# Kernel tuning notes

Measured on AMD Instinct MI355X. Metric: run time of the kernel, lower is better.

Reference implementation:

```python
import jax, jax.numpy as jnp
import numpy as np

C = 256
NH = 8
G = 32  # groupnorm groups (min(32, C))
EPS = 1e-6


def setup_inputs() -> dict:
    key = jax.random.key(0)
    ks = jax.random.split(key, 7)
    B, D, H, W = 2, 16, 16, 16
    x = jax.random.normal(ks[0], (B, C, D, H, W), dtype=jnp.float32)
    gn_gamma = jnp.ones((C,), jnp.float32)
    gn_beta = jnp.zeros((C,), jnp.float32)
    s = 1.0 / np.sqrt(C)
    qkv_w = jax.random.normal(ks[1], (3 * C, C), jnp.float32) * s  # 1x1x1 conv weight
    qkv_b = jnp.zeros((3 * C,), jnp.float32)
    proj_w = jax.random.normal(ks[2], (C, C), jnp.float32) * s
    proj_b = jnp.zeros((C,), jnp.float32)
    return {"x": x, "gn_gamma": gn_gamma, "gn_beta": gn_beta,
            "qkv_w": qkv_w, "qkv_b": qkv_b, "proj_w": proj_w, "proj_b": proj_b}


def _group_norm(x, gamma, beta):
    # x: [B, C, S]
    B, Cc, S = x.shape
    xg = x.reshape(B, G, (Cc // G) * S)
    mu = xg.mean(axis=-1, keepdims=True)
    var = xg.var(axis=-1, keepdims=True)
    xg = (xg - mu) * jax.lax.rsqrt(var + EPS)
    x = xg.reshape(B, Cc, S)
    return x * gamma[None, :, None] + beta[None, :, None]


def reference(x, gn_gamma, gn_beta, qkv_w, qkv_b, proj_w, proj_b):
    B, Cc, D, H, W = x.shape
    S = D * H * W
    hd = Cc // NH
    xf = x.reshape(B, Cc, S)
    h = _group_norm(xf, gn_gamma, gn_beta)
    # 1x1x1 conv == channel matmul: [B, 3C, S]
    qkv = jnp.einsum('oc,bcs->bos', qkv_w, h) + qkv_b[None, :, None]
    # torch path: reshape(B,3C,S).permute(0,2,1).chunk -> q=channels[0:C]
    q, k, v = qkv[:, :Cc], qkv[:, Cc:2 * Cc], qkv[:, 2 * Cc:]
    # [B, C, S] -> [B, NH, S, hd]
    def to_heads(t):
        return t.reshape(B, NH, hd, S).transpose(0, 1, 3, 2)
    q, k, v = to_heads(q), to_heads(k), to_heads(v)
    scale = hd ** (-0.5)
    attn = jax.nn.softmax(jnp.einsum('bnqd,bnkd->bnqk', q, k) * scale, axis=-1)
    o = jnp.einsum('bnqk,bnkd->bnqd', attn, v)  # [B, NH, S, hd]
    o = o.transpose(0, 1, 3, 2).reshape(B, Cc, S)  # back to [B, C, S]
    o = jnp.einsum('oc,bcs->bos', proj_w, o) + proj_b[None, :, None]
    return x + o.reshape(B, Cc, D, H, W)
```

## Files before the change

kernel.cpp:

```cpp
#include <hip/hip_runtime.h>
#include <cstddef>

#define S_LEN 4096
#define C_DIM 256
#define NHEADS 8
#define HDIM 32

typedef __attribute__((ext_vector_type(8))) _Float16 half8;
typedef __attribute__((ext_vector_type(4))) _Float16 half4;
typedef __attribute__((ext_vector_type(2))) _Float16 h2t;
typedef __attribute__((ext_vector_type(2))) __fp16 fp16x2;
typedef __attribute__((ext_vector_type(4))) float floatx4;

#define SC2F ((float)(0.17677669529663687 * 1.4426950408889634))

__global__ __launch_bounds__(256) void prep_stats(
    const float* __restrict__ qkv_w, const float* __restrict__ proj_w,
    const float* __restrict__ qkv_b, const float* __restrict__ x,
    _Float16* __restrict__ wq, _Float16* __restrict__ wp,
    float* __restrict__ qbias, float* __restrict__ pstat)
{
  const int blk = blockIdx.x;
  const int tid = threadIdx.x;
  if (blk < 512) {
    __shared__ float red[2][4];
    const int gb = blk >> 3, e = blk & 7;
    const int g = gb & 31, b = gb >> 5;
    const float* xb = x + ((size_t)b * C_DIM + g * 8) * S_LEN + e * 4096;
    const float4* x4 = (const float4*)xb;
    float sum = 0.f, sumsq = 0.f;
    #pragma unroll
    for (int i = 0; i < 4; ++i) {
      float4 v = x4[tid + i * 256];
      sum += v.x + v.y + v.z + v.w;
      sumsq += v.x * v.x + v.y * v.y + v.z * v.z + v.w * v.w;
    }
    for (int off = 1; off < 64; off <<= 1) {
      sum += __shfl_xor(sum, off, 64);
      sumsq += __shfl_xor(sumsq, off, 64);
    }
    const int wv = tid >> 6, lane = tid & 63;
    if (lane == 0) { red[0][wv] = sum; red[1][wv] = sumsq; }
    __syncthreads();
    if (tid == 0) {
      pstat[(gb * 8 + e) * 2 + 0] = red[0][0] + red[0][1] + red[0][2] + red[0][3];
      pstat[(gb * 8 + e) * 2 + 1] = red[1][0] + red[1][1] + red[1][2] + red[1][3];
    }
  } else {
    int idx = (blk - 512) * 256 + tid;
    if (idx < 768 * 256) {
      float v = qkv_w[idx];
      if (idx < 256 * 256) v *= SC2F;
      wq[idx] = (_Float16)v;
    } else if (idx < 768 * 256 + 256 * 256) {
      int i = idx - 768 * 256;
      wp[i] = (_Float16)proj_w[i];
    } else if (idx < 768 * 256 + 256 * 256 + 768) {
      int i = idx - (768 * 256 + 256 * 256);
      float bv = qkv_b[i];
      if (i < 256) bv *= SC2F;
      qbias[i] = bv;
    }
  }
}

__global__ __launch_bounds__(256) void qkv_gn_gemm(
    const _Float16* __restrict__ W, const float* __restrict__ bias,
    const float* __restrict__ x, const float* __restrict__ gamma,
    const float* __restrict__ beta, const float* __restrict__ pstat,
    _Float16* __restrict__ qo, _Float16* __restrict__ ko_,
    _Float16* __restrict__ vo)
{
  __shared__ __align__(16) _Float16 Ld[64 * 264];
  const int tid = threadIdx.x;
  const int b = blockIdx.z;
  const int s0 = blockIdx.y * 64;

  {
    const int c0 = (tid & 127) * 2, c1 = c0 + 1;
    const int sh = tid >> 7;
    const int g = c0 >> 3;
    const int gb = b * 32 + g;
    float s = 0.f, sq = 0.f;
    #pragma unroll
    for (int e = 0; e < 8; ++e) {
      s  += pstat[(gb * 8 + e) * 2 + 0];
      sq += pstat[(gb * 8 + e) * 2 + 1];
    }
    const float mean = s * (1.f / 32768.f);
    const float rstd = rsqrtf(sq * (1.f / 32768.f) - mean * mean + 1e-6f);
    const float ga0 = gamma[c0] * rstd, be0 = beta[c0] - mean * ga0;
    const float ga1 = gamma[c1] * rstd, be1 = beta[c1] - mean * ga1;
    const float4* xa = (const float4*)(x + ((size_t)b * C_DIM + c0) * S_LEN + s0 + sh * 32);
    const float4* xc = (const float4*)(x + ((size_t)b * C_DIM + c1) * S_LEN + s0 + sh * 32);
    #pragma unroll
    for (int j = 0; j < 8; ++j) {
      float4 a = xa[j], c = xc[j];
      int sl = sh * 32 + j * 4;
      *(h2t*)&Ld[(sl + 0) * 264 + c0] = (h2t){ (_Float16)(a.x * ga0 + be0), (_Float16)(c.x * ga1 + be1) };
      *(h2t*)&Ld[(sl + 1) * 264 + c0] = (h2t){ (_Float16)(a.y * ga0 + be0), (_Float16)(c.y * ga1 + be1) };
      *(h2t*)&Ld[(sl + 2) * 264 + c0] = (h2t){ (_Float16)(a.z * ga0 + be0), (_Float16)(c.z * ga1 + be1) };
      *(h2t*)&Ld[(sl + 3) * 264 + c0] = (h2t){ (_Float16)(a.w * ga0 + be0), (_Float16)(c.w * ga1 + be1) };
    }
  }
  __syncthreads();

  const int lane = tid & 63, wv = tid >> 6;
  const int m = lane & 15, quad = lane >> 4;
  const int mtb = blockIdx.x * 8 + wv * 2;
  const _Float16* wrow0 = W + (size_t)((mtb + 0) * 16 + m) * C_DIM + quad * 8;
  const _Float16* wrow1 = W + (size_t)((mtb + 1) * 16 + m) * C_DIM + quad * 8;
  const _Float16* lp = &Ld[m * 264 + quad * 8];

  floatx4 acc[2][4];
  #pragma unroll
  for (int j = 0; j < 2; ++j)
    #pragma unroll
    for (int s = 0; s < 4; ++s) acc[j][s] = (floatx4){0.f,0.f,0.f,0.f};

  #pragma unroll
  for (int k0 = 0; k0 < C_DIM; k0 += 32) {
    half8 b0 = *(const half8*)(lp + k0);
    half8 b1 = *(const half8*)(lp + 16 * 264 + k0);
    half8 b2 = *(const half8*)(lp + 32 * 264 + k0);
    half8 b3 = *(const half8*)(lp + 48 * 264 + k0);
    half8 a0 = *(const half8*)(wrow0 + k0);
    half8 a1 = *(const half8*)(wrow1 + k0);
    acc[0][0] = __builtin_amdgcn_mfma_f32_16x16x32_f16(a0, b0, acc[0][0], 0, 0, 0);
    acc[0][1] = __builtin_amdgcn_mfma_f32_16x16x32_f16(a0, b1, acc[0][1], 0, 0, 0);
    acc[0][2] = __builtin_amdgcn_mfma_f32_16x16x32_f16(a0, b2, acc[0][2], 0, 0, 0);
    acc[0][3] = __builtin_amdgcn_mfma_f32_16x16x32_f16(a0, b3, acc[0][3], 0, 0, 0);
    acc[1][0] = __builtin_amdgcn_mfma_f32_16x16x32_f16(a1, b0, acc[1][0], 0, 0, 0);
    acc[1][1] = __builtin_amdgcn_mfma_f32_16x16x32_f16(a1, b1, acc[1][1], 0, 0, 0);
    acc[1][2] = __builtin_amdgcn_mfma_f32_16x16x32_f16(a1, b2, acc[1][2], 0, 0, 0);
    acc[1][3] = __builtin_amdgcn_mfma_f32_16x16x32_f16(a1, b3, acc[1][3], 0, 0, 0);
  }

  if (blockIdx.x < 4) {
    #pragma unroll
    for (int j = 0; j < 2; ++j) {
      const int ob = (mtb + j) * 16 + quad * 4;
      const float bv0 = bias[ob], bv1 = bias[ob + 1],
                  bv2 = bias[ob + 2], bv3 = bias[ob + 3];
      #pragma unroll
      for (int sub = 0; sub < 4; ++sub) {
        int s = s0 + sub * 16 + m;
        half4 h = { (_Float16)(acc[j][sub][0] + bv0), (_Float16)(acc[j][sub][1] + bv1),
                    (_Float16)(acc[j][sub][2] + bv2), (_Float16)(acc[j][sub][3] + bv3) };
        _Float16* dst = (ob < 256) ? qo : ko_;
        int oo = ob & 255, n = oo >> 5, d0 = oo & 31;
        *(half4*)(dst + (((size_t)b * NHEADS + n) * S_LEN + s) * HDIM + d0) = h;
      }
    }
  } else {
    __syncthreads();
    _Float16* VLd = Ld;
    #pragma unroll
    for (int j = 0; j < 2; ++j) {
      const int ob = (mtb + j) * 16 + quad * 4;
      const int lch = (wv * 2 + j) * 16 + quad * 4;
      const float bv0 = bias[ob], bv1 = bias[ob + 1],
                  bv2 = bias[ob + 2], bv3 = bias[ob + 3];
      #pragma unroll
      for (int sub = 0; sub < 4; ++sub) {
        int s = sub * 16 + m;
        VLd[(lch + 0) * 72 + s] = (_Float16)(acc[j][sub][0] + bv0);
        VLd[(lch + 1) * 72 + s] = (_Float16)(acc[j][sub][1] + bv1);
        VLd[(lch + 2) * 72 + s] = (_Float16)(acc[j][sub][2] + bv2);
        VLd[(lch + 3) * 72 + s] = (_Float16)(acc[j][sub][3] + bv3);
      }
    }
    __syncthreads();
    const int lch = tid >> 1, sh = tid & 1;
    const int oo = (blockIdx.x - 4) * 128 + lch;
    const int n = oo >> 5, d = oo & 31;
    _Float16* dst = vo + ((size_t)(b * NHEADS + n) * HDIM + d) * S_LEN + s0 + sh * 32;
    const _Float16* src = VLd + lch * 72 + sh * 32;
    *(half8*)(dst + 0)  = *(const half8*)(src + 0);
    *(half8*)(dst + 8)  = *(const half8*)(src + 8);
    *(half8*)(dst + 16) = *(const half8*)(src + 16);
    *(half8*)(dst + 24) = *(const half8*)(src + 24);
  }
}

__global__ __launch_bounds__(512) void attn_kernel(
    const _Float16* __restrict__ q, const _Float16* __restrict__ k,
    const _Float16* __restrict__ v, _Float16* __restrict__ po,
    float* __restrict__ pl)
{
  __shared__ __align__(16) _Float16 Kl[2][128 * 40];
  __shared__ __align__(16) _Float16 Vl[2][32 * 136];
  const int tid = threadIdx.x;
  const int lane = tid & 63, wv = tid >> 6;
  const int m = lane & 15, quad = lane >> 4;
  const int n = blockIdx.y, b = blockIdx.z;
  const int qc = blockIdx.x >> 1, kh = blockIdx.x & 1;
  const int q0 = qc * 256 + wv * 32;
  const int bh = b * NHEADS + n;

  const _Float16* qb = q + (size_t)bh * S_LEN * HDIM;
  const _Float16* kb = k + (size_t)bh * S_LEN * HDIM + (size_t)kh * 2048 * HDIM;
  const _Float16* vb = v + (size_t)bh * HDIM * S_LEN + (size_t)kh * 2048;

  half8 qfA = *(const half8*)(qb + (size_t)(q0 + m) * HDIM + quad * 8);
  half8 qfB = *(const half8*)(qb + (size_t)(q0 + 16 + m) * HDIM + quad * 8);

  const int krow = wv * 16 + (lane >> 2), kc = (lane & 3) * 8;
  const int vrow = wv * 4 + (lane >> 4), vc = (lane & 15) * 8;
  const _Float16* kg = kb + (size_t)krow * HDIM + kc;
  const _Float16* vg = vb + (size_t)vrow * S_LEN + vc;
  const int klds = krow * 40 + kc;
  const int vlds = vrow * 136 + vc;

  int4 kreg = *(const int4*)kg;
  int4 vreg = *(const int4*)vg;
  const _Float16* kgp = kg + 128 * HDIM;
  const _Float16* vgp = vg + 128;

  floatx4 oA0 = {0.f,0.f,0.f,0.f}, oA1 = oA0, oB0 = oA0, oB1 = oA0;
  float lA0 = 0.f, lA1 = 0.f, lB0 = 0.f, lB1 = 0.f;
  const fp16x2 one2 = { (__fp16)1.0f, (__fp16)1.0f };
  const floatx4 zz = {0.f,0.f,0.f,0.f};

  #pragma unroll 2
  for (int it = 0; it < 16; ++it) {
    const int bufi = it & 1;
    *(int4*)(&Kl[bufi][klds]) = kreg;
    *(int4*)(&Vl[bufi][vlds]) = vreg;
    kreg = *(const int4*)kgp; kgp += 128 * HDIM;
    vreg = *(const int4*)vgp; vgp += 128;
    __syncthreads();
    const _Float16* Kb = Kl[bufi];
    const _Float16* Vb = Vl[bufi];

    #pragma unroll
    for (int t = 0; t < 8; ++t) {
      const int tt = (t + wv) & 7;
      half8 kf  = *(const half8*)(Kb + (tt * 16 + m) * 40 + quad * 8);
      half4 vf0 = *(const half4*)(Vb + m * 136 + tt * 16 + quad * 4);
      half4 vf1 = *(const half4*)(Vb + (16 + m) * 136 + tt * 16 + quad * 4);
      __builtin_amdgcn_s_setprio(1);
      floatx4 sA = __builtin_amdgcn_mfma_f32_16x16x32_f16(kf, qfA, zz, 0, 0, 0);
      floatx4 sB = __builtin_amdgcn_mfma_f32_16x16x32_f16(kf, qfB, zz, 0, 0, 0);
      __builtin_amdgcn_s_setprio(0);
      float eA0 = __builtin_amdgcn_exp2f(sA[0]);
      float eA1 = __builtin_amdgcn_exp2f(sA[1]);
      float eA2 = __builtin_amdgcn_exp2f(sA[2]);
      float eA3 = __builtin_amdgcn_exp2f(sA[3]);
      float eB0 = __builtin_amdgcn_exp2f(sB[0]);
      float eB1 = __builtin_amdgcn_exp2f(sB[1]);
      float eB2 = __builtin_amdgcn_exp2f(sB[2]);
      float eB3 = __builtin_amdgcn_exp2f(sB[3]);
      half4 pA, pB;
      fp16x2 pAlo = __builtin_amdgcn_cvt_pkrtz(eA0, eA1);
      fp16x2 pAhi = __builtin_amdgcn_cvt_pkrtz(eA2, eA3);
      fp16x2 pBlo = __builtin_amdgcn_cvt_pkrtz(eB0, eB1);
      fp16x2 pBhi = __builtin_amdgcn_cvt_pkrtz(eB2, eB3);
      *(fp16x2*)&pA = pAlo; *((fp16x2*)&pA + 1) = pAhi;
      *(fp16x2*)&pB = pBlo; *((fp16x2*)&pB + 1) = pBhi;
      lA0 = __builtin_amdgcn_fdot2(pAlo, one2, lA0, false);
      lA1 = __builtin_amdgcn_fdot2(pAhi, one2, lA1, false);
      lB0 = __builtin_amdgcn_fdot2(pBlo, one2, lB0, false);
      lB1 = __builtin_amdgcn_fdot2(pBhi, one2, lB1, false);
      __builtin_amdgcn_s_setprio(1);
      oA0 = __builtin_amdgcn_mfma_f32_16x16x16f16(vf0, pA, oA0, 0, 0, 0);
      oA1 = __builtin_amdgcn_mfma_f32_16x16x16f16(vf1, pA, oA1, 0, 0, 0);
      oB0 = __builtin_amdgcn_mfma_f32_16x16x16f16(vf0, pB, oB0, 0, 0, 0);
      oB1 = __builtin_amdgcn_mfma_f32_16x16x16f16(vf1, pB, oB1, 0, 0, 0);
      __builtin_amdgcn_s_setprio(0);
    }
  }
  float lA = lA0 + lA1, lB = lB0 + lB1;
  lA += __shfl_xor(lA, 16, 64); lA += __shfl_xor(lA, 32, 64);
  lB += __shfl_xor(lB, 16, 64); lB += __shfl_xor(lB, 32, 64);
  _Float16* pobase = po + (size_t)kh * 2097152 + ((size_t)bh * S_LEN) * HDIM;
  {
    _Float16* poh = pobase + (size_t)(q0 + m) * HDIM;
    half4 h0 = { (_Float16)oA0[0], (_Float16)oA0[1], (_Float16)oA0[2], (_Float16)oA0[3] };
    half4 h1 = { (_Float16)oA1[0], (_Float16)oA1[1], (_Float16)oA1[2], (_Float16)oA1[3] };
    *(half4*)(poh + quad * 4) = h0;
    *(half4*)(poh + 16 + quad * 4) = h1;
    if (quad == 0) pl[(size_t)kh * 65536 + (size_t)bh * S_LEN + q0 + m] = lA;
  }
  {
    _Float16* poh = pobase + (size_t)(q0 + 16 + m) * HDIM;
    half4 h0 = { (_Float16)oB0[0], (_Float16)oB0[1], (_Float16)oB0[2], (_Float16)oB0[3] };
    half4 h1 = { (_Float16)oB1[0], (_Float16)oB1[1], (_Float16)oB1[2], (_Float16)oB1[3] };
    *(half4*)(poh + quad * 4) = h0;
    *(half4*)(poh + 16 + quad * 4) = h1;
    if (quad == 0) pl[(size_t)kh * 65536 + (size_t)bh * S_LEN + q0 + 16 + m] = lB;
  }
}

__global__ __launch_bounds__(256) void proj_gemm(
    const _Float16* __restrict__ W, const float* __restrict__ bias,
    const _Float16* __restrict__ po, const float* __restrict__ pl,
    const float* __restrict__ x, float* __restrict__ out)
{
  __shared__ float Linv[512];
  const int tid = threadIdx.x;
  const int lane = tid & 63, wv = tid >> 6;
  const int m = lane & 15, quad = lane >> 4;
  const int mt = blockIdx.x * 4 + wv;
  const int s0 = blockIdx.y * 64;
  const int b = blockIdx.z;
  const int row = mt * 16 + m;

  {
    const int nn = tid >> 5, jj = (tid & 31) * 2;
    size_t base = (size_t)(b * NHEADS + nn) * S_LEN + s0 + jj;
    float a0 = pl[base]     + pl[65536 + base];
    float a1 = pl[base + 1] + pl[65536 + base + 1];
    Linv[nn * 64 + jj]     = 1.f / a0;
    Linv[nn * 64 + jj + 1] = 1.f / a1;
  }
  __syncthreads();

  const _Float16* wrow = W + (size_t)row * C_DIM + quad * 8;
  floatx4 acc0 = {0.f,0.f,0.f,0.f}, acc1 = acc0, acc2 = acc0, acc3 = acc0;
  #pragma unroll
  for (int k0 = 0; k0 < C_DIM; k0 += 32) {
    const int n = k0 >> 5;
    const int d0 = quad * 8;
    half8 bf[4];
    #pragma unroll
    for (int sub = 0; sub < 4; ++sub) {
      size_t idx = (((size_t)(b * NHEADS + n)) * S_LEN + s0 + sub * 16 + m) * HDIM + d0;
      half8 a = *(const half8*)(po + idx);
      half8 c = *(const half8*)(po + 2097152 + idx);
      _Float16 iv = (_Float16)Linv[n * 64 + sub * 16 + m];
      bf[sub] = (a + c) * iv;
    }
    half8 af = *(const half8*)(wrow + k0);
    acc0 = __builtin_amdgcn_mfma_f32_16x16x32_f16(af, bf[0], acc0, 0, 0, 0);
    acc1 = __builtin_amdgcn_mfma_f32_16x16x32_f16(af, bf[1], acc1, 0, 0, 0);
    acc2 = __builtin_amdgcn_mfma_f32_16x16x32_f16(af, bf[2], acc2, 0, 0, 0);
    acc3 = __builtin_amdgcn_mfma_f32_16x16x32_f16(af, bf[3], acc3, 0, 0, 0);
  }
  floatx4 accs[4] = {acc0, acc1, acc2, acc3};
  #pragma unroll
  for (int sub = 0; sub < 4; ++sub) {
    int s = s0 + sub * 16 + m;
    #pragma unroll
    for (int r = 0; r < 4; ++r) {
      int c = mt * 16 + quad * 4 + r;
      size_t idx = ((size_t)b * C_DIM + c) * S_LEN + s;
      out[idx] = x[idx] + accs[sub][r] + bias[c];
    }
  }
}

extern "C" void kernel_launch(void* const* d_in, const int* in_sizes, int n_in,
                              void* d_out, int out_size, void* d_ws, size_t ws_size,
                              hipStream_t stream) {
  const float* x        = (const float*)d_in[0];
  const float* gn_gamma = (const float*)d_in[1];
  const float* gn_beta  = (const float*)d_in[2];
  const float* qkv_w    = (const float*)d_in[3];
  const float* qkv_b    = (const float*)d_in[4];
  const float* proj_w   = (const float*)d_in[5];
  const float* proj_b   = (const float*)d_in[6];
  float* out = (float*)d_out;

  const size_t n1 = (size_t)2 * S_LEN * C_DIM;
  char* ws = (char*)d_ws;
  _Float16* qx  = (_Float16*)ws;
  _Float16* kx  = qx + n1;
  _Float16* vx  = kx + n1;
  _Float16* wq  = vx + n1;
  _Float16* wp  = wq + 768 * 256;
  float*    qbias = (float*)(wp + 256 * 256);
  float*    pstat = qbias + 768;
  _Float16* po  = (_Float16*)(pstat + 1024);
  float*    pl  = (float*)(po + 2 * n1);

  prep_stats<<<1539, 256, 0, stream>>>(qkv_w, proj_w, qkv_b, x, wq, wp, qbias, pstat);
  qkv_gn_gemm<<<dim3(6, 64, 2), 256, 0, stream>>>(wq, qbias, x, gn_gamma, gn_beta, pstat, qx, kx, vx);
  attn_kernel<<<dim3(32, 8, 2), 512, 0, stream>>>(qx, kx, vx, po, pl);
  proj_gemm<<<dim3(4, 64, 2), 256, 0, stream>>>(wp, proj_b, po, pl, x, out);
}
```

Baseline: 148.3 us.

## Split GroupNorm into a transpose kernel and widen the QKV and proj GEMM tiles

GroupNorm normalisation and the fp16 transpose move into a new xnorm kernel that writes an [S,C] fp16 buffer. The QKV GEMM then only copies that buffer into LDS and computes 64 output rows per wave, halving its x-dimension grid. The output projection also doubles rows per wave, so each loaded po tile is reused across two weight tiles. The aim is to cut the redundant per-block recomputation of the normalised input (previously repeated in six blocks per tile) and to improve operand reuse. The cost is an extra kernel launch, a global round trip for the normalised activations, and fewer blocks with higher register pressure in both GEMMs.

```diff
diff --git a/kernel.cpp b/kernel.cpp
--- a/kernel.cpp
+++ b/kernel.cpp
@@ -64,91 +64,108 @@
   }
 }
 
-__global__ __launch_bounds__(256) void qkv_gn_gemm(
-    const _Float16* __restrict__ W, const float* __restrict__ bias,
+__global__ __launch_bounds__(256) void xnorm(
     const float* __restrict__ x, const float* __restrict__ gamma,
     const float* __restrict__ beta, const float* __restrict__ pstat,
+    _Float16* __restrict__ xt)
+{
+  __shared__ _Float16 Lt[16][264];
+  const int tid = threadIdx.x;
+  const int b = blockIdx.y;
+  const int s0 = blockIdx.x * 16;
+  const int c = tid;
+  const int gb = b * 32 + (c >> 3);
+  float s = 0.f, sq = 0.f;
+  #pragma unroll
+  for (int e = 0; e < 8; ++e) {
+    s  += pstat[(gb * 8 + e) * 2 + 0];
+    sq += pstat[(gb * 8 + e) * 2 + 1];
+  }
+  const float mean = s * (1.f / 32768.f);
+  const float rstd = rsqrtf(sq * (1.f / 32768.f) - mean * mean + 1e-6f);
+  const float ga = gamma[c] * rstd, be = beta[c] - mean * ga;
+  const float4* xa = (const float4*)(x + ((size_t)b * C_DIM + c) * S_LEN + s0);
+  #pragma unroll
+  for (int i = 0; i < 4; ++i) {
+    float4 v = xa[i];
+    Lt[i * 4 + 0][c] = (_Float16)(v.x * ga + be);
+    Lt[i * 4 + 1][c] = (_Float16)(v.y * ga + be);
+    Lt[i * 4 + 2][c] = (_Float16)(v.z * ga + be);
+    Lt[i * 4 + 3][c] = (_Float16)(v.w * ga + be);
+  }
+  __syncthreads();
+  const int sl = tid >> 4, cc = (tid & 15) * 16;
+  _Float16* dst = xt + ((size_t)b * S_LEN + s0 + sl) * C_DIM + cc;
+  const _Float16* src = &Lt[sl][cc];
+  *(half8*)(dst + 0) = *(const half8*)(src + 0);
+  *(half8*)(dst + 8) = *(const half8*)(src + 8);
+}
+
+__global__ __launch_bounds__(256) void qkv_gemm(
+    const _Float16* __restrict__ W, const float* __restrict__ bias,
+    const _Float16* __restrict__ xt,
     _Float16* __restrict__ qo, _Float16* __restrict__ ko_,
     _Float16* __restrict__ vo)
 {
-  __shared__ __align__(16) _Float16 Ld[64 * 264];
+  __shared__ __align__(16) _Float16 Ld[256 * 72];
   const int tid = threadIdx.x;
   const int b = blockIdx.z;
   const int s0 = blockIdx.y * 64;
 
   {
-    const int c0 = (tid & 127) * 2, c1 = c0 + 1;
-    const int sh = tid >> 7;
-    const int g = c0 >> 3;
-    const int gb = b * 32 + g;
-    float s = 0.f, sq = 0.f;
-    #pragma unroll
-    for (int e = 0; e < 8; ++e) {
-      s  += pstat[(gb * 8 + e) * 2 + 0];
-      sq += pstat[(gb * 8 + e) * 2 + 1];
-    }
-    const float mean = s * (1.f / 32768.f);
-    const float rstd = rsqrtf(sq * (1.f / 32768.f) - mean * mean + 1e-6f);
-    const float ga0 = gamma[c0] * rstd, be0 = beta[c0] - mean * ga0;
-    const float ga1 = gamma[c1] * rstd, be1 = beta[c1] - mean * ga1;
-    const float4* xa = (const float4*)(x + ((size_t)b * C_DIM + c0) * S_LEN + s0 + sh * 32);
-    const float4* xc = (const float4*)(x + ((size_t)b * C_DIM + c1) * S_LEN + s0 + sh * 32);
-    #pragma unroll
-    for (int j = 0; j < 8; ++j) {
-      float4 a = xa[j], c = xc[j];
-      int sl = sh * 32 + j * 4;
-      *(h2t*)&Ld[(sl + 0) * 264 + c0] = (h2t){ (_Float16)(a.x * ga0 + be0), (_Float16)(c.x * ga1 + be1) };
-      *(h2t*)&Ld[(sl + 1) * 264 + c0] = (h2t){ (_Float16)(a.y * ga0 + be0), (_Float16)(c.y * ga1 + be1) };
-      *(h2t*)&Ld[(sl + 2) * 264 + c0] = (h2t){ (_Float16)(a.z * ga0 + be0), (_Float16)(c.z * ga1 + be1) };
-      *(h2t*)&Ld[(sl + 3) * 264 + c0] = (h2t){ (_Float16)(a.w * ga0 + be0), (_Float16)(c.w * ga1 + be1) };
-    }
+    const int sl = tid >> 2, cc = (tid & 3) * 64;
+    const _Float16* src = xt + ((size_t)b * S_LEN + s0 + sl) * C_DIM + cc;
+    _Float16* dst = &Ld[sl * 264 + cc];
+    #pragma unroll
+    for (int j = 0; j < 8; ++j)
+      *(half8*)(dst + j * 8) = *(const half8*)(src + j * 8);
   }
   __syncthreads();
 
   const int lane = tid & 63, wv = tid >> 6;
   const int m = lane & 15, quad = lane >> 4;
-  const int mtb = blockIdx.x * 8 + wv * 2;
-  const _Float16* wrow0 = W + (size_t)((mtb + 0) * 16 + m) * C_DIM + quad * 8;
-  const _Float16* wrow1 = W + (size_t)((mtb + 1) * 16 + m) * C_DIM + quad * 8;
+  const int mtb = blockIdx.x * 16 + wv * 4;
+  const _Float16* wrow[4];
+  #pragma unroll
+  for (int j = 0; j < 4; ++j)
+    wrow[j] = W + (size_t)((mtb + j) * 16 + m) * C_DIM + quad * 8;
   const _Float16* lp = &Ld[m * 264 + quad * 8];
 
-  floatx4 acc[2][4];
-  #pragma unroll
-  for (int j = 0; j < 2; ++j)
+  floatx4 acc[4][4];
+  #pragma unroll
+  for (int j = 0; j < 4; ++j)
     #pragma unroll
     for (int s = 0; s < 4; ++s) acc[j][s] = (floatx4){0.f,0.f,0.f,0.f};
 
-  #pragma unroll
+  #pragma unroll 2
   for (int k0 = 0; k0 < C_DIM; k0 += 32) {
     half8 b0 = *(const half8*)(lp + k0);
     half8 b1 = *(const half8*)(lp + 16 * 264 + k0);
     half8 b2 = *(const half8*)(lp + 32 * 264 + k0);
     half8 b3 = *(const half8*)(lp + 48 * 264 + k0);
-    half8 a0 = *(const half8*)(wrow0 + k0);
-    half8 a1 = *(const half8*)(wrow1 + k0);
-    acc[0][0] = __builtin_amdgcn_mfma_f32_16x16x32_f16(a0, b0, acc[0][0], 0, 0, 0);
-    acc[0][1] = __builtin_amdgcn_mfma_f32_16x16x32_f16(a0, b1, acc[0][1], 0, 0, 0);
-    acc[0][2] = __builtin_amdgcn_mfma_f32_16x16x32_f16(a0, b2, acc[0][2], 0, 0, 0);
-    acc[0][3] = __builtin_amdgcn_mfma_f32_16x16x32_f16(a0, b3, acc[0][3], 0, 0, 0);
-    acc[1][0] = __builtin_amdgcn_mfma_f32_16x16x32_f16(a1, b0, acc[1][0], 0, 0, 0);
-    acc[1][1] = __builtin_amdgcn_mfma_f32_16x16x32_f16(a1, b1, acc[1][1], 0, 0, 0);
-    acc[1][2] = __builtin_amdgcn_mfma_f32_16x16x32_f16(a1, b2, acc[1][2], 0, 0, 0);
-    acc[1][3] = __builtin_amdgcn_mfma_f32_16x16x32_f16(a1, b3, acc[1][3], 0, 0, 0);
-  }
-
-  if (blockIdx.x < 4) {
-    #pragma unroll
-    for (int j = 0; j < 2; ++j) {
+    #pragma unroll
+    for (int j = 0; j < 4; ++j) {
+      half8 a = *(const half8*)(wrow[j] + k0);
+      acc[j][0] = __builtin_amdgcn_mfma_f32_16x16x32_f16(a, b0, acc[j][0], 0, 0, 0);
+      acc[j][1] = __builtin_amdgcn_mfma_f32_16x16x32_f16(a, b1, acc[j][1], 0, 0, 0);
+      acc[j][2] = __builtin_amdgcn_mfma_f32_16x16x32_f16(a, b2, acc[j][2], 0, 0, 0);
+      acc[j][3] = __builtin_amdgcn_mfma_f32_16x16x32_f16(a, b3, acc[j][3], 0, 0, 0);
+    }
+  }
+
+  if (blockIdx.x < 2) {
+    #pragma unroll
+    for (int j = 0; j < 4; ++j) {
       const int ob = (mtb + j) * 16 + quad * 4;
       const float bv0 = bias[ob], bv1 = bias[ob + 1],
                   bv2 = bias[ob + 2], bv3 = bias[ob + 3];
+      _Float16* dst = (ob < 256) ? qo : ko_;
+      const int oo = ob & 255, n = oo >> 5, d0 = oo & 31;
       #pragma unroll
       for (int sub = 0; sub < 4; ++sub) {
         int s = s0 + sub * 16 + m;
         half4 h = { (_Float16)(acc[j][sub][0] + bv0), (_Float16)(acc[j][sub][1] + bv1),
                     (_Float16)(acc[j][sub][2] + bv2), (_Float16)(acc[j][sub][3] + bv3) };
-        _Float16* dst = (ob < 256) ? qo : ko_;
-        int oo = ob & 255, n = oo >> 5, d0 = oo & 31;
         *(half4*)(dst + (((size_t)b * NHEADS + n) * S_LEN + s) * HDIM + d0) = h;
       }
     }
@@ -156,9 +173,9 @@
     __syncthreads();
     _Float16* VLd = Ld;
     #pragma unroll
-    for (int j = 0; j < 2; ++j) {
+    for (int j = 0; j < 4; ++j) {
       const int ob = (mtb + j) * 16 + quad * 4;
-      const int lch = (wv * 2 + j) * 16 + quad * 4;
+      const int lch = (wv * 4 + j) * 16 + quad * 4;
       const float bv0 = bias[ob], bv1 = bias[ob + 1],
                   bv2 = bias[ob + 2], bv3 = bias[ob + 3];
       #pragma unroll
@@ -171,15 +188,14 @@
       }
     }
     __syncthreads();
-    const int lch = tid >> 1, sh = tid & 1;
-    const int oo = (blockIdx.x - 4) * 128 + lch;
-    const int n = oo >> 5, d = oo & 31;
-    _Float16* dst = vo + ((size_t)(b * NHEADS + n) * HDIM + d) * S_LEN + s0 + sh * 32;
-    const _Float16* src = VLd + lch * 72 + sh * 32;
-    *(half8*)(dst + 0)  = *(const half8*)(src + 0);
-    *(half8*)(dst + 8)  = *(const half8*)(src + 8);
-    *(half8*)(dst + 16) = *(const half8*)(src + 16);
-    *(half8*)(dst + 24) = *(const half8*)(src + 24);
+    const int sh3 = tid & 7, chl = tid >> 3;
+    #pragma unroll
+    for (int p = 0; p < 8; ++p) {
+      const int ch = p * 32 + chl;
+      const int n = ch >> 5, d = ch & 31;
+      _Float16* dst = vo + ((size_t)(b * NHEADS + n) * HDIM + d) * S_LEN + s0 + sh3 * 8;
+      *(half8*)dst = *(const half8*)(VLd + ch * 72 + sh3 * 8);
+    }
   }
 }
 
@@ -301,10 +317,9 @@
   const int tid = threadIdx.x;
   const int lane = tid & 63, wv = tid >> 6;
   const int m = lane & 15, quad = lane >> 4;
-  const int mt = blockIdx.x * 4 + wv;
+  const int mtb = blockIdx.x * 8 + wv * 2;
   const int s0 = blockIdx.y * 64;
   const int b = blockIdx.z;
-  const int row = mt * 16 + m;
 
   {
     const int nn = tid >> 5, jj = (tid & 31) * 2;
@@ -316,8 +331,14 @@
   }
   __syncthreads();
 
-  const _Float16* wrow = W + (size_t)row * C_DIM + quad * 8;
-  floatx4 acc0 = {0.f,0.f,0.f,0.f}, acc1 = acc0, acc2 = acc0, acc3 = acc0;
+  const _Float16* wrow0 = W + (size_t)((mtb + 0) * 16 + m) * C_DIM + quad * 8;
+  const _Float16* wrow1 = W + (size_t)((mtb + 1) * 16 + m) * C_DIM + quad * 8;
+  floatx4 acc[2][4];
+  #pragma unroll
+  for (int j = 0; j < 2; ++j)
+    #pragma unroll
+    for (int s = 0; s < 4; ++s) acc[j][s] = (floatx4){0.f,0.f,0.f,0.f};
+
   #pragma unroll
   for (int k0 = 0; k0 < C_DIM; k0 += 32) {
     const int n = k0 >> 5;
@@ -331,23 +352,26 @@
       _Float16 iv = (_Float16)Linv[n * 64 + sub * 16 + m];
       bf[sub] = (a + c) * iv;
     }
-    half8 af = *(const half8*)(wrow + k0);
-    acc0 = __builtin_amdgcn_mfma_f32_16x16x32_f16(af, bf[0], acc0, 0, 0, 0);
-    acc1 = __builtin_amdgcn_mfma_f32_16x16x32_f16(af, bf[1], acc1, 0, 0, 0);
-    acc2 = __builtin_amdgcn_mfma_f32_16x16x32_f16(af, bf[2], acc2, 0, 0, 0);
-    acc3 = __builtin_amdgcn_mfma_f32_16x16x32_f16(af, bf[3], acc3, 0, 0, 0);
-  }
-  floatx4 accs[4] = {acc0, acc1, acc2, acc3};
-  #pragma unroll
-  for (int sub = 0; sub < 4; ++sub) {
-    int s = s0 + sub * 16 + m;
-    #pragma unroll
-    for (int r = 0; r < 4; ++r) {
-      int c = mt * 16 + quad * 4 + r;
-      size_t idx = ((size_t)b * C_DIM + c) * S_LEN + s;
-      out[idx] = x[idx] + accs[sub][r] + bias[c];
-    }
-  }
+    half8 af0 = *(const half8*)(wrow0 + k0);
+    half8 af1 = *(const half8*)(wrow1 + k0);
+    #pragma unroll
+    for (int sub = 0; sub < 4; ++sub) {
+      acc[0][sub] = __builtin_amdgcn_mfma_f32_16x16x32_f16(af0, bf[sub], acc[0][sub], 0, 0, 0);
+      acc[1][sub] = __builtin_amdgcn_mfma_f32_16x16x32_f16(af1, bf[sub], acc[1][sub], 0, 0, 0);
+    }
+  }
+  #pragma unroll
+  for (int j = 0; j < 2; ++j)
+    #pragma unroll
+    for (int sub = 0; sub < 4; ++sub) {
+      int s = s0 + sub * 16 + m;
+      #pragma unroll
+      for (int r = 0; r < 4; ++r) {
+        int c = (mtb + j) * 16 + quad * 4 + r;
+        size_t idx = ((size_t)b * C_DIM + c) * S_LEN + s;
+        out[idx] = x[idx] + acc[j][sub][r] + bias[c];
+      }
+    }
 }
 
 extern "C" void kernel_launch(void* const* d_in, const int* in_sizes, int n_in,
@@ -373,9 +397,11 @@
   float*    pstat = qbias + 768;
   _Float16* po  = (_Float16*)(pstat + 1024);
   float*    pl  = (float*)(po + 2 * n1);
+  _Float16* xt  = (_Float16*)(pl + 2 * 65536);
 
   prep_stats<<<1539, 256, 0, stream>>>(qkv_w, proj_w, qkv_b, x, wq, wp, qbias, pstat);
-  qkv_gn_gemm<<<dim3(6, 64, 2), 256, 0, stream>>>(wq, qbias, x, gn_gamma, gn_beta, pstat, qx, kx, vx);
+  xnorm<<<dim3(256, 2), 256, 0, stream>>>(x, gn_gamma, gn_beta, pstat, xt);
+  qkv_gemm<<<dim3(3, 64, 2), 256, 0, stream>>>(wq, qbias, xt, qx, kx, vx);
   attn_kernel<<<dim3(32, 8, 2), 512, 0, stream>>>(qx, kx, vx, po, pl);
-  proj_gemm<<<dim3(4, 64, 2), 256, 0, stream>>>(wp, proj_b, po, pl, x, out);
-}
+  proj_gemm<<<dim3(2, 64, 2), 256, 0, stream>>>(wp, proj_b, po, pl, x, out);
+}
```

Result: faster. 144.0 us (-2.9%).
